# Kernel tuning notes

Measured on AMD Instinct MI355X. Metric: run time of the kernel, lower is better.

Reference implementation:

```python
import jax, jax.numpy as jnp
import numpy as np
import math

HIDDEN = 1024
NUM_HEADS = 16
HEAD_DIM = HIDDEN // NUM_HEADS
BIAS_SCALE = 1.0
ROPE_BASE = 10000.0


def rotate_half(x):
    h = x.shape[-1] // 2
    return jnp.concatenate([-x[..., h:], x[..., :h]], axis=-1)


def rope_cos_sin(seq_len, dim):
    inv_freq = 1.0 / (ROPE_BASE ** (jnp.arange(0, dim, 2, dtype=jnp.float32) / dim))
    t = jnp.arange(seq_len, dtype=jnp.float32)
    freqs = jnp.einsum('i,j->ij', t, inv_freq)          # [S, dim/2]
    emb = jnp.concatenate([freqs, freqs], axis=-1)       # [S, dim]
    return jnp.cos(emb), jnp.sin(emb)


def setup_inputs() -> dict:
    key = jax.random.key(0)
    ks = jax.random.split(key, 6)
    B, S = 2, 2048
    x = jax.random.normal(ks[0], (B, S, HIDDEN), dtype=jnp.float32)
    attention_mask = jnp.ones((B, S), dtype=jnp.int32)
    # xavier-uniform-like init for the four projections (Linear, bias=False)
    limit = math.sqrt(6.0 / (HIDDEN + HIDDEN))
    Wq = jax.random.uniform(ks[1], (HIDDEN, HIDDEN), jnp.float32, -limit, limit)
    Wk = jax.random.uniform(ks[2], (HIDDEN, HIDDEN), jnp.float32, -limit, limit)
    Wv = jax.random.uniform(ks[3], (HIDDEN, HIDDEN), jnp.float32, -limit, limit)
    Wo = jax.random.uniform(ks[4], (HIDDEN, HIDDEN), jnp.float32, -limit, limit)
    # learnable contextual bias, tril'd at init per _init_weights
    cb = jax.random.normal(ks[5], (S, S), dtype=jnp.float32) * 0.02
    contextual_bias = jnp.tril(cb)
    return {"x": x, "attention_mask": attention_mask, "Wq": Wq, "Wk": Wk,
            "Wv": Wv, "Wo": Wo, "contextual_bias": contextual_bias}


def reference(x, attention_mask, Wq, Wk, Wv, Wo, contextual_bias):
    B, S, H = x.shape
    nh, hd = NUM_HEADS, HEAD_DIM
    # projections (torch Linear: y = x @ W^T)
    q = (x @ Wq.T).reshape(B, S, nh, hd)
    k = (x @ Wk.T).reshape(B, S, nh, hd)
    v = (x @ Wv.T).reshape(B, S, nh, hd)
    # RoPE (applied per position along seq dim)
    cos, sin = rope_cos_sin(S, hd)                       # [S, hd]
    cos = cos[None, :, None, :]
    sin = sin[None, :, None, :]
    q = q * cos + rotate_half(q) * sin
    k = k * cos + rotate_half(k) * sin
    q = q.transpose(0, 2, 1, 3)                          # [B, nh, S, hd]
    k = k.transpose(0, 2, 1, 3)
    v = v.transpose(0, 2, 1, 3)
    scores = jnp.einsum('bhqd,bhkd->bhqk', q, k) / math.sqrt(hd)
    scores = scores + contextual_bias[None, None] * BIAS_SCALE
    # padding mask over key dim
    pad = (attention_mask == 0)[:, None, None, :]        # [B,1,1,S]
    scores = jnp.where(pad, -jnp.inf, scores)
    # causal mask
    causal = jnp.triu(jnp.ones((S, S), dtype=bool), k=1)
    scores = jnp.where(causal[None, None], -jnp.inf, scores)
    attn = jax.nn.softmax(scores, axis=-1)               # dropout: eval mode (identity)
    out = jnp.einsum('bhqk,bhkd->bhqd', attn, v)
    out = out.transpose(0, 2, 1, 3).reshape(B, S, H)
    output = out @ Wo.T
    return output, attn
```

## Files before the change

kernel.cpp:

```cpp
#include <hip/hip_runtime.h>
#include <hip/hip_bf16.h>
#include <math.h>

#define S_LEN 2048
#define HID   1024
#define NH    16
#define HD    64
#define BATCH 2

typedef __bf16 bf16;
typedef __attribute__((ext_vector_type(4))) __bf16 bf16x4;
typedef __attribute__((ext_vector_type(8))) __bf16 bf16x8;
typedef __attribute__((ext_vector_type(4))) float f32x4;

__global__ __launch_bounds__(256) void cvt_f32_bf16(
    const float* __restrict__ src, bf16* __restrict__ dst, int n)
{
    int stride = gridDim.x * 256 * 4;
    for (int i = (blockIdx.x * 256 + threadIdx.x) * 4; i < n; i += stride) {
        float4 v = *(const float4*)(src + i);
        bf16x4 o;
        o[0] = (bf16)v.x; o[1] = (bf16)v.y; o[2] = (bf16)v.z; o[3] = (bf16)v.w;
        *(bf16x4*)(dst + i) = o;
    }
}

__global__ __launch_bounds__(256) void rope_tab(float2* __restrict__ tab)
{
    int i = blockIdx.x * 256 + threadIdx.x;
    int sp = i >> 5, d = i & 31;
    float f = (float)sp * exp2f(-(float)d * (13.287712379549449f / 32.0f));
    float sn, cs;
    sincosf(f, &sn, &cs);
    tab[i] = make_float2(cs, sn);
}

#define BM 128
#define BN 128
#define BK 64

__device__ __forceinline__ void gload_lds16(const void* g, void* l) {
    __builtin_amdgcn_global_load_lds(
        (__attribute__((address_space(1))) void*)g,
        (__attribute__((address_space(3))) void*)l, 16, 0, 0);
}

template <int MODE>
__global__ __launch_bounds__(512) void gemm_bf16(
    const bf16* __restrict__ A, const bf16* __restrict__ W,
    void* __restrict__ Cout, const float2* __restrict__ rope,
    int M, int N, int K)
{
    __shared__ bf16 As[BM * BK];
    __shared__ bf16 Bs[BN * BK];

    const int tid  = threadIdx.x;
    const int lane = tid & 63;
    const int w    = tid >> 6;
    const int wr   = w >> 2;
    const int wc   = w & 3;
    const int m0   = blockIdx.x * BM;
    const int n0   = blockIdx.y * BN;
    const int fr   = lane & 15;
    const int fq   = lane >> 4;
    const int nb   = ((wc >> 1) << 6) + ((wc & 1) << 4);

    const int i0 = tid, i1 = tid + 512;
    const int r0 = i0 >> 3, c0 = i0 & 7, g0 = c0 ^ (r0 & 7);
    const int r1 = i1 >> 3, c1 = i1 & 7, g1 = c1 ^ (r1 & 7);
    const bf16* Ag0 = A + (size_t)(m0 + r0) * K + g0 * 8;
    const bf16* Ag1 = A + (size_t)(m0 + r1) * K + g1 * 8;
    const bf16* Wg0 = W + (size_t)(n0 + r0) * K + g0 * 8;
    const bf16* Wg1 = W + (size_t)(n0 + r1) * K + g1 * 8;
    bf16* Al0 = As + i0 * 8;
    bf16* Al1 = As + i1 * 8;
    bf16* Bl0 = Bs + i0 * 8;
    bf16* Bl1 = Bs + i1 * 8;
    const char* As_b = (const char*)As;
    const char* Bs_b = (const char*)Bs;

    f32x4 acc[4][2];
    #pragma unroll
    for (int mi = 0; mi < 4; ++mi)
        #pragma unroll
        for (int nj = 0; nj < 2; ++nj)
            acc[mi][nj] = (f32x4){0.f, 0.f, 0.f, 0.f};

    for (int k0 = 0; k0 < K; k0 += BK) {
        gload_lds16(Ag0 + k0, Al0);
        gload_lds16(Ag1 + k0, Al1);
        gload_lds16(Wg0 + k0, Bl0);
        gload_lds16(Wg1 + k0, Bl1);
        asm volatile("s_waitcnt vmcnt(0)" ::: "memory");
        __syncthreads();

        bf16x8 af[4][2], bw[2][2];
        #pragma unroll
        for (int mi = 0; mi < 4; ++mi) {
            int mrow = wr * 64 + mi * 16 + fr;
            #pragma unroll
            for (int kk = 0; kk < 2; ++kk) {
                int ch = (kk * 4 + fq) ^ (mrow & 7);
                af[mi][kk] = *(const bf16x8*)(As_b + mrow * 128 + ch * 16);
            }
        }
        #pragma unroll
        for (int nj = 0; nj < 2; ++nj) {
            int nrow = nb + nj * 32 + fr;
            #pragma unroll
            for (int kk = 0; kk < 2; ++kk) {
                int ch = (kk * 4 + fq) ^ (nrow & 7);
                bw[nj][kk] = *(const bf16x8*)(Bs_b + nrow * 128 + ch * 16);
            }
        }
        #pragma unroll
        for (int kk = 0; kk < 2; ++kk)
            #pragma unroll
            for (int mi = 0; mi < 4; ++mi)
                #pragma unroll
                for (int nj = 0; nj < 2; ++nj)
                    acc[mi][nj] = __builtin_amdgcn_mfma_f32_16x16x32_bf16(
                        af[mi][kk], bw[nj][kk], acc[mi][nj], 0, 0, 0);
        __syncthreads();
    }

    if (MODE == 0) {
        float* C = (float*)Cout;
        #pragma unroll
        for (int mi = 0; mi < 4; ++mi) {
            #pragma unroll
            for (int r = 0; r < 4; ++r) {
                int m = m0 + wr * 64 + mi * 16 + fq * 4 + r;
                #pragma unroll
                for (int nj = 0; nj < 2; ++nj) {
                    int n = n0 + nb + nj * 32 + fr;
                    C[(size_t)m * N + n] = acc[mi][nj][r];
                }
            }
        }
    } else {
        bf16* C = (bf16*)Cout;
        const int h = (n0 >> 6) + (wc >> 1);
        const int dlo = ((wc & 1) << 4) + fr;
        #pragma unroll
        for (int mi = 0; mi < 4; ++mi) {
            #pragma unroll
            for (int r = 0; r < 4; ++r) {
                int m  = m0 + wr * 64 + mi * 16 + fq * 4 + r;
                int b  = m >> 11;
                int sp = m & (S_LEN - 1);
                size_t base = (((size_t)b * NH + h) * S_LEN + sp) * HD;
                if (MODE == 2) {
                    #pragma unroll
                    for (int nj = 0; nj < 2; ++nj)
                        C[base + dlo + nj * 32] = (bf16)acc[mi][nj][r];
                } else {
                    float2 t = rope[(size_t)sp * 32 + dlo];
                    float lo = acc[mi][0][r], hi = acc[mi][1][r];
                    C[base + dlo]      = (bf16)(lo * t.x - hi * t.y);
                    C[base + dlo + 32] = (bf16)(hi * t.x + lo * t.y);
                }
            }
        }
    }
}

#define SC_PITCH 2052

__global__ __launch_bounds__(256) void attn_mfma(
    const bf16* __restrict__ Qt, const bf16* __restrict__ Kt,
    const bf16* __restrict__ Vt, const float* __restrict__ bias,
    const int* __restrict__ mask, float* __restrict__ attn,
    bf16* __restrict__ ho)
{
    extern __shared__ char smem[];
    float* sc     = (float*)smem;
    float* red    = sc + 16 * SC_PITCH;
    float* rowmax = red + 256;
    float* invl   = rowmax + 16;

    const int tid  = threadIdx.x;
    const int lane = tid & 63;
    const int w    = tid >> 6;
    const int n    = lane & 15;
    const int quad = lane >> 4;

    const int qt = 127 - blockIdx.x;
    const int bh = blockIdx.y;
    const int b  = bh >> 4, h = bh & 15;
    const int q0 = qt * 16;
    const int ncols = q0 + 16;
    const int T = qt + 1;

    const bf16* qbase = Qt + ((size_t)bh * S_LEN + q0 + n) * HD + quad * 8;
    bf16x8 qf0 = *(const bf16x8*)(qbase);
    bf16x8 qf1 = *(const bf16x8*)(qbase + 32);

    const int* mrow = mask + b * S_LEN;

    for (int t = w; t < T; t += 4) {
        int k0 = t * 16;
        int krow = k0 + n;
        const bf16* kbase = Kt + ((size_t)bh * S_LEN + krow) * HD + quad * 8;
        bf16x8 b0 = *(const bf16x8*)(kbase);
        bf16x8 b1 = *(const bf16x8*)(kbase + 32);
        f32x4 c = {0.f, 0.f, 0.f, 0.f};
        c = __builtin_amdgcn_mfma_f32_16x16x32_bf16(qf0, b0, c, 0, 0, 0);
        c = __builtin_amdgcn_mfma_f32_16x16x32_bf16(qf1, b1, c, 0, 0, 0);
        int mk = mrow[krow];
        #pragma unroll
        for (int r = 0; r < 4; ++r) {
            int qr = quad * 4 + r;
            int qabs = q0 + qr;
            float s = c[r] * 0.125f + bias[(size_t)qabs * S_LEN + krow];
            if (krow > qabs || mk == 0) s = -3.0e38f;
            sc[qr * SC_PITCH + krow] = s;
        }
    }
    __syncthreads();

    {
        const int r = tid & 15, s_id = tid >> 4;
        float lmax = -3.0e38f;
        for (int c = s_id; c < ncols; c += 16)
            lmax = fmaxf(lmax, sc[r * SC_PITCH + c]);
        red[tid] = lmax;
        __syncthreads();
        #pragma unroll
        for (int st = 128; st >= 16; st >>= 1) {
            if (tid < st) red[tid] = fmaxf(red[tid], red[tid + st]);
            __syncthreads();
        }
        if (tid < 16) rowmax[tid] = red[tid];
        __syncthreads();

        float mx = rowmax[r];
        float lsum = 0.f;
        for (int c = s_id; c < ncols; c += 16) {
            float p = __expf(sc[r * SC_PITCH + c] - mx);
            sc[r * SC_PITCH + c] = p;
            lsum += p;
        }
        red[tid] = lsum;
        __syncthreads();
        #pragma unroll
        for (int st = 128; st >= 16; st >>= 1) {
            if (tid < st) red[tid] += red[tid + st];
            __syncthreads();
        }
        if (tid < 16) invl[tid] = 1.0f / red[tid];
        __syncthreads();
    }

    for (int r2 = 0; r2 < 16; ++r2) {
        float iv = invl[r2];
        float* arow = attn + ((size_t)bh * S_LEN + q0 + r2) * S_LEN;
        for (int c = tid * 4; c < S_LEN; c += 1024) {
            float4 o;
            if (c < ncols) {
                const float* s4 = sc + r2 * SC_PITCH + c;
                o.x = s4[0] * iv; o.y = s4[1] * iv;
                o.z = s4[2] * iv; o.w = s4[3] * iv;
            } else {
                o.x = o.y = o.z = o.w = 0.f;
            }
            *(float4*)(arow + c) = o;
        }
    }

    {
        const int d = w * 16 + n;
        const int m = n;
        f32x4 acc0 = {0.f, 0.f, 0.f, 0.f};
        f32x4 acc1 = {0.f, 0.f, 0.f, 0.f};
        int toggle = 0;
        for (int kc = 0; kc < ncols; kc += 32, toggle ^= 1) {
            bf16x8 af, vf;
            #pragma unroll
            for (int j = 0; j < 8; ++j) {
                int k = kc + quad * 8 + j;
                float pv = (k < ncols) ? sc[m * SC_PITCH + k] : 0.f;
                af[j] = (bf16)pv;
                vf[j] = Vt[((size_t)bh * S_LEN + k) * HD + d];
            }
            if (toggle == 0)
                acc0 = __builtin_amdgcn_mfma_f32_16x16x32_bf16(af, vf, acc0, 0, 0, 0);
            else
                acc1 = __builtin_amdgcn_mfma_f32_16x16x32_bf16(af, vf, acc1, 0, 0, 0);
        }
        #pragma unroll
        for (int r = 0; r < 4; ++r) {
            int qr = quad * 4 + r;
            float o = (acc0[r] + acc1[r]) * invl[qr];
            ho[((size_t)(b * S_LEN + q0 + qr)) * HID + h * HD + d] = (bf16)o;
        }
    }
}

extern "C" void kernel_launch(void* const* d_in, const int* in_sizes, int n_in,
                              void* d_out, int out_size, void* d_ws, size_t ws_size,
                              hipStream_t stream) {
    const float* x     = (const float*)d_in[0];
    const int*   mask  = (const int*)d_in[1];
    const float* Wq    = (const float*)d_in[2];
    const float* Wk    = (const float*)d_in[3];
    const float* Wv    = (const float*)d_in[4];
    const float* Wo    = (const float*)d_in[5];
    const float* cbias = (const float*)d_in[6];

    float* out  = (float*)d_out;
    float* attn = out + (size_t)BATCH * S_LEN * HID;

    const size_t QKV = (size_t)BATCH * S_LEN * HID;
    const size_t WEL = (size_t)HID * HID;
    bf16* Qt  = (bf16*)d_ws;
    bf16* Kt  = Qt + QKV;
    bf16* Vt  = Kt + QKV;
    bf16* Xb  = Vt + QKV;
    bf16* Wqb = Xb + QKV;
    bf16* Wkb = Wqb + WEL;
    bf16* Wvb = Wkb + WEL;
    bf16* Wob = Wvb + WEL;
    bf16* Ho  = Xb;
    float2* rope = (float2*)out;

    const int M = BATCH * S_LEN;

    cvt_f32_bf16<<<2048, 256, 0, stream>>>(x, Xb, (int)QKV);
    cvt_f32_bf16<<<1024, 256, 0, stream>>>(Wq, Wqb, (int)WEL);
    cvt_f32_bf16<<<1024, 256, 0, stream>>>(Wk, Wkb, (int)WEL);
    cvt_f32_bf16<<<1024, 256, 0, stream>>>(Wv, Wvb, (int)WEL);
    cvt_f32_bf16<<<1024, 256, 0, stream>>>(Wo, Wob, (int)WEL);
    rope_tab<<<256, 256, 0, stream>>>(rope);

    dim3 g(M / BM, HID / BN), blk(512);
    gemm_bf16<1><<<g, blk, 0, stream>>>(Xb, Wqb, Qt, rope, M, HID, HID);
    gemm_bf16<1><<<g, blk, 0, stream>>>(Xb, Wkb, Kt, rope, M, HID, HID);
    gemm_bf16<2><<<g, blk, 0, stream>>>(Xb, Wvb, Vt, nullptr, M, HID, HID);

    const size_t lds_bytes = (16 * SC_PITCH + 256 + 32) * sizeof(float);
    static bool attr_set = false;
    if (!attr_set) {
        hipFuncSetAttribute((const void*)attn_mfma,
                            hipFuncAttributeMaxDynamicSharedMemorySize,
                            (int)lds_bytes);
        attr_set = true;
    }
    attn_mfma<<<dim3(S_LEN / 16, BATCH * NH), dim3(256), lds_bytes, stream>>>(
        Qt, Kt, Vt, cbias, mask, attn, Ho);

    gemm_bf16<0><<<g, blk, 0, stream>>>(Ho, Wob, out, nullptr, M, HID, HID);
}
```

Measured before the change: 1.290 ms.

## Store V transposed per head so PV loads are contiguous vector reads

The V projection epilogue now stages its tile in shared memory and writes V as [B,NH,HD,S], so each head-dim row is contiguous along the sequence. The attention PV loop then loads eight consecutive bf16 values as one vector instead of eight strided scalar gathers. This cuts global load instructions and uncoalesced traffic in the attention kernel. In exchange the projection adds a shared-memory transpose and an extra barrier, and the loads may read V past ncols, where they are multiplied by zero probabilities.

```diff
diff --git a/kernel.cpp b/kernel.cpp
--- a/kernel.cpp
+++ b/kernel.cpp
@@ -124,7 +124,7 @@
         __syncthreads();
     }
 
-    if (MODE == 0) {
+    if constexpr (MODE == 0) {
         float* C = (float*)Cout;
         #pragma unroll
         for (int mi = 0; mi < 4; ++mi) {
@@ -138,7 +138,7 @@
                 }
             }
         }
-    } else {
+    } else if constexpr (MODE == 1) {
         bf16* C = (bf16*)Cout;
         const int h = (n0 >> 6) + (wc >> 1);
         const int dlo = ((wc & 1) << 4) + fr;
@@ -150,18 +150,38 @@
                 int b  = m >> 11;
                 int sp = m & (S_LEN - 1);
                 size_t base = (((size_t)b * NH + h) * S_LEN + sp) * HD;
-                if (MODE == 2) {
-                    #pragma unroll
-                    for (int nj = 0; nj < 2; ++nj)
-                        C[base + dlo + nj * 32] = (bf16)acc[mi][nj][r];
-                } else {
-                    float2 t = rope[(size_t)sp * 32 + dlo];
-                    float lo = acc[mi][0][r], hi = acc[mi][1][r];
-                    C[base + dlo]      = (bf16)(lo * t.x - hi * t.y);
-                    C[base + dlo + 32] = (bf16)(hi * t.x + lo * t.y);
+                float2 t = rope[(size_t)sp * 32 + dlo];
+                float lo = acc[mi][0][r], hi = acc[mi][1][r];
+                C[base + dlo]      = (bf16)(lo * t.x - hi * t.y);
+                C[base + dlo + 32] = (bf16)(hi * t.x + lo * t.y);
+            }
+        }
+    } else {
+        __shared__ __align__(16) bf16 sT[128 * 136];
+        #pragma unroll
+        for (int mi = 0; mi < 4; ++mi) {
+            #pragma unroll
+            for (int r = 0; r < 4; ++r) {
+                int ml = wr * 64 + mi * 16 + fq * 4 + r;
+                #pragma unroll
+                for (int nj = 0; nj < 2; ++nj) {
+                    int nl = nb + nj * 32 + fr;
+                    sT[nl * 136 + ml] = (bf16)acc[mi][nj][r];
                 }
             }
         }
+        __syncthreads();
+        int dl  = tid >> 2;
+        int seg = (tid & 3) * 32;
+        int bb  = m0 >> 11;
+        int spg = (m0 & (S_LEN - 1)) + seg;
+        int hh  = (n0 >> 6) + (dl >> 6);
+        int dd  = dl & 63;
+        bf16* dst = (bf16*)Cout + ((size_t)(bb * NH + hh) * HD + dd) * S_LEN + spg;
+        const bf16* srcp = sT + dl * 136 + seg;
+        #pragma unroll
+        for (int i = 0; i < 4; ++i)
+            *(bf16x8*)(dst + i * 8) = *(const bf16x8*)(srcp + i * 8);
     }
 }
 
@@ -169,7 +189,7 @@
 
 __global__ __launch_bounds__(256) void attn_mfma(
     const bf16* __restrict__ Qt, const bf16* __restrict__ Kt,
-    const bf16* __restrict__ Vt, const float* __restrict__ bias,
+    const bf16* __restrict__ VT, const float* __restrict__ bias,
     const int* __restrict__ mask, float* __restrict__ attn,
     bf16* __restrict__ ho)
 {
@@ -271,17 +291,18 @@
     {
         const int d = w * 16 + n;
         const int m = n;
+        const bf16* vrow = VT + ((size_t)bh * HD + d) * S_LEN;
         f32x4 acc0 = {0.f, 0.f, 0.f, 0.f};
         f32x4 acc1 = {0.f, 0.f, 0.f, 0.f};
         int toggle = 0;
         for (int kc = 0; kc < ncols; kc += 32, toggle ^= 1) {
-            bf16x8 af, vf;
+            bf16x8 af;
+            bf16x8 vf = *(const bf16x8*)(vrow + kc + quad * 8);
             #pragma unroll
             for (int j = 0; j < 8; ++j) {
                 int k = kc + quad * 8 + j;
                 float pv = (k < ncols) ? sc[m * SC_PITCH + k] : 0.f;
                 af[j] = (bf16)pv;
-                vf[j] = Vt[((size_t)bh * S_LEN + k) * HD + d];
             }
             if (toggle == 0)
                 acc0 = __builtin_amdgcn_mfma_f32_16x16x32_bf16(af, vf, acc0, 0, 0, 0);
```

Result: faster. 1.196 ms (-7.3%).
